# Performance work log

Hardware: AMD Instinct MI355X
Metric: run time of the kernel (lower is better)

## Reference

```python
import jax, jax.numpy as jnp
import numpy as np
from jax import lax

IN_CH = 256
FILTERS_PER_CH = 2            # expansion = 1 -> 2 filters per input channel
INTER_CH = IN_CH * FILTERS_PER_CH
BUTTERFLY_SIZE = 8
BUTTERFLIES = INTER_CH // 2 // BUTTERFLY_SIZE  # 32
WING = BUTTERFLY_SIZE // 2                      # 4


def setup_inputs() -> dict:
    key = jax.random.key(0)
    k1, k2 = jax.random.split(key)
    x = jax.random.normal(k1, (32, IN_CH, 56, 56), dtype=jnp.float32)
    # depthwise conv weight, PyTorch OIHW with groups=IN_CH: (INTER_CH, 1, 3, 3)
    w = jax.random.normal(k2, (INTER_CH, 1, 3, 3), dtype=jnp.float32) * 0.1
    return {"x": x, "w": w}


def reference(x, w):
    # grouped (depthwise, channel multiplier 2) conv, stride 1, pad 1, no bias
    y = lax.conv_general_dilated(
        x, w,
        window_strides=(1, 1),
        padding=[(1, 1), (1, 1)],
        feature_group_count=IN_CH,
        dimension_numbers=("NCHW", "OIHW", "NCHW"),
    )  # (B, INTER_CH, H, W); channels group-major: 2i,2i+1 from input i
    B, C2, H, W = y.shape
    # extract_sequences: consecutive channels alternate between the two outputs
    y = y.reshape(B, C2 // 2, 2, H, W)
    x1 = y[:, :, 0]  # (B, IN_CH, H, W)
    x2 = y[:, :, 1]
    # swap_wings: within each butterfly, swap the two wings
    s = x2.reshape(B, BUTTERFLIES, 2, WING, H, W)
    x2 = jnp.flip(s, axis=2).reshape(B, C2 // 2, H, W)
    return x1 + x2
```

## Files before the change

### kernel.cpp

```cpp
#include <hip/hip_runtime.h>

#define IN_CH 256
#define IMG_W 56
typedef float f4 __attribute__((ext_vector_type(4)));

__global__ __launch_bounds__(448, 5) void dwconv_butterfly(
    const float* __restrict__ x, const float* __restrict__ wgt,
    float* __restrict__ out)
{
    const int tid = threadIdx.x;
    const int pb  = blockIdx.x;
    const int p   = pb & 127;
    const int b   = pb >> 7;
    const int c0  = ((p >> 2) << 3) | (p & 3);
    const int c1  = c0 ^ 4;

    const size_t chan = (size_t)IMG_W * IMG_W;
    const float* x0 = x + ((size_t)b * IN_CH + c0) * chan;
    const float* x1 = x + ((size_t)b * IN_CH + c1) * chan;
    float* o0 = out + ((size_t)b * IN_CH + c0) * chan;
    float* o1 = out + ((size_t)b * IN_CH + c1) * chan;

    const float* pwa = wgt + (size_t)(2 * c0) * 9;
    const float* pwb = wgt + (size_t)(2 * c1 + 1) * 9;
    const float* pwc = wgt + (size_t)(2 * c1) * 9;
    const float* pwd = wgt + (size_t)(2 * c0 + 1) * 9;
    float wa[9], wb[9], wc[9], wd[9];
#pragma unroll
    for (int i = 0; i < 9; ++i) {
        wa[i] = pwa[i]; wb[i] = pwb[i]; wc[i] = pwc[i]; wd[i] = pwd[i];
    }

    if (tid >= 392) return;
    const int s  = tid % 14;
    const int rp = tid / 14;
    const int w0 = 4 * s;
    const bool has_l = (s > 0), has_r = (s < 13);
    const int  col_l = has_l ? w0 - 1 : 0;
    const int  col_r = has_r ? w0 + 4 : IMG_W - 1;

    f4    va[4], vb[4];
    float la[4], ra[4], lb[4], rb[4];
    bool  rv[4];
#pragma unroll
    for (int k = 0; k < 4; ++k) {
        const int ir  = 2 * rp - 1 + k;
        rv[k] = (unsigned)ir < 56u;
        const int irc = ir < 0 ? 0 : (ir > 55 ? 55 : ir);
        const float* r0 = x0 + irc * IMG_W;
        const float* r1 = x1 + irc * IMG_W;
        va[k] = *(const f4*)(r0 + w0);
        vb[k] = *(const f4*)(r1 + w0);
        la[k] = r0[col_l];
        ra[k] = r0[col_r];
        lb[k] = r1[col_l];
        rb[k] = r1[col_r];
    }

    float acc[2][8];
#pragma unroll
    for (int j = 0; j < 2; ++j)
#pragma unroll
        for (int i = 0; i < 8; ++i) acc[j][i] = 0.f;

#pragma unroll
    for (int k = 0; k < 4; ++k) {
        const bool z = !rv[k];
        float W0[6], W1[6];
        W0[0] = (z || !has_l) ? 0.f : la[k];
        W0[1] = z ? 0.f : va[k].x;  W0[2] = z ? 0.f : va[k].y;
        W0[3] = z ? 0.f : va[k].z;  W0[4] = z ? 0.f : va[k].w;
        W0[5] = (z || !has_r) ? 0.f : ra[k];
        W1[0] = (z || !has_l) ? 0.f : lb[k];
        W1[1] = z ? 0.f : vb[k].x;  W1[2] = z ? 0.f : vb[k].y;
        W1[3] = z ? 0.f : vb[k].z;  W1[4] = z ? 0.f : vb[k].w;
        W1[5] = (z || !has_r) ? 0.f : rb[k];
#pragma unroll
        for (int j = 0; j < 2; ++j) {
            const int kh = k - j;
            if (kh < 0 || kh > 2) continue;
#pragma unroll
            for (int kw = 0; kw < 3; ++kw) {
                const float fa = wa[kh * 3 + kw], fb = wb[kh * 3 + kw];
                const float fc = wc[kh * 3 + kw], fd = wd[kh * 3 + kw];
#pragma unroll
                for (int i = 0; i < 4; ++i) {
                    const float u0 = W0[i + kw];
                    const float u1 = W1[i + kw];
                    acc[j][i]     += u0 * fa + u1 * fb;
                    acc[j][4 + i] += u1 * fc + u0 * fd;
                }
            }
        }
    }

#pragma unroll
    for (int j = 0; j < 2; ++j) {
        const int orow = 2 * rp + j;
        f4 v0; v0.x = acc[j][0]; v0.y = acc[j][1]; v0.z = acc[j][2]; v0.w = acc[j][3];
        f4 v1; v1.x = acc[j][4]; v1.y = acc[j][5]; v1.z = acc[j][6]; v1.w = acc[j][7];
        *(f4*)(o0 + orow * IMG_W + w0) = v0;
        *(f4*)(o1 + orow * IMG_W + w0) = v1;
    }
}

extern "C" void kernel_launch(void* const* d_in, const int* in_sizes, int n_in,
                              void* d_out, int out_size, void* d_ws, size_t ws_size,
                              hipStream_t stream) {
    const float* x = (const float*)d_in[0];
    const float* w = (const float*)d_in[1];
    float* out = (float*)d_out;

    dim3 grid(128 * 32);
    dim3 block(448);
    dwconv_butterfly<<<grid, block, 0, stream>>>(x, w, out);
}
```

Baseline: 195.2 us.

## Make waves persistent with double-buffered loads and shuffle-based halo exchange

Each wavefront now handles an 8-row strip of a channel pair and loops over 7 such tiles, prefetching the next tile's inputs and weights into a second register set while computing the current one. The per-thread left and right halo scalar loads are replaced by cross-lane shuffles of neighbouring f4 values. The grid drops to 1024 blocks of 256 threads. The goal is fewer global loads and less block-launch overhead, with load latency overlapping compute. The cost is higher register pressure from the two buffers, 8 of 64 lanes idle per wave, and fewer resident waves to hide latency.

```diff
diff --git a/kernel.cpp b/kernel.cpp
--- a/kernel.cpp
+++ b/kernel.cpp
@@ -2,105 +2,136 @@
 
 #define IN_CH 256
 #define IMG_W 56
+#define CHF   3136
 typedef float f4 __attribute__((ext_vector_type(4)));
 
-__global__ __launch_bounds__(448, 5) void dwconv_butterfly(
+__global__ __launch_bounds__(256, 4) void dwconv_butterfly(
     const float* __restrict__ x, const float* __restrict__ wgt,
     float* __restrict__ out)
 {
-    const int tid = threadIdx.x;
-    const int pb  = blockIdx.x;
-    const int p   = pb & 127;
-    const int b   = pb >> 7;
-    const int c0  = ((p >> 2) << 3) | (p & 3);
-    const int c1  = c0 ^ 4;
+    const int lane = threadIdx.x & 63;
+    const int widx = __builtin_amdgcn_readfirstlane(threadIdx.x >> 6);
+    const int gw   = blockIdx.x * 4 + widx;
+    const int r    = lane / 14;
+    const int s    = lane - r * 14;
+    const bool act   = lane < 56;
+    const int  w0    = 4 * s;
+    const bool has_l = (s > 0), has_r = (s < 13);
 
-    const size_t chan = (size_t)IMG_W * IMG_W;
-    const float* x0 = x + ((size_t)b * IN_CH + c0) * chan;
-    const float* x1 = x + ((size_t)b * IN_CH + c1) * chan;
-    float* o0 = out + ((size_t)b * IN_CH + c0) * chan;
-    float* o1 = out + ((size_t)b * IN_CH + c1) * chan;
+    auto LOAD = [&](int t, f4* va, f4* vb, float* w4) {
+        const int jt = gw + 4096 * t;
+        const int q  = jt % 7;
+        const int pb = jt / 7;
+        const int p  = pb & 127;
+        const int b  = pb >> 7;
+        const int c0 = ((p >> 2) << 3) | (p & 3);
+        const int c1 = c0 ^ 4;
+        const float* x0 = x + ((size_t)b * IN_CH + c0) * CHF;
+        const float* x1 = x + ((size_t)b * IN_CH + c1) * CHF;
+        const int brow = 8 * q + 2 * r - 1;
+        if (act) {
+#pragma unroll
+            for (int k = 0; k < 4; ++k) {
+                const int ir  = brow + k;
+                const int irc = ir < 0 ? 0 : (ir > 55 ? 55 : ir);
+                va[k] = *(const f4*)(x0 + irc * IMG_W + w0);
+                vb[k] = *(const f4*)(x1 + irc * IMG_W + w0);
+            }
+        }
+        const float* pa = wgt + (size_t)(2 * c0) * 9;
+        const float* pq = wgt + (size_t)(2 * c1 + 1) * 9;
+        const float* pc = wgt + (size_t)(2 * c1) * 9;
+        const float* pd = wgt + (size_t)(2 * c0 + 1) * 9;
+#pragma unroll
+        for (int i = 0; i < 9; ++i) {
+            w4[i] = pa[i]; w4[9 + i] = pq[i]; w4[18 + i] = pc[i]; w4[27 + i] = pd[i];
+        }
+    };
 
-    const float* pwa = wgt + (size_t)(2 * c0) * 9;
-    const float* pwb = wgt + (size_t)(2 * c1 + 1) * 9;
-    const float* pwc = wgt + (size_t)(2 * c1) * 9;
-    const float* pwd = wgt + (size_t)(2 * c0 + 1) * 9;
-    float wa[9], wb[9], wc[9], wd[9];
+    auto COMPUTE = [&](int t, f4* va, f4* vb, const float* w4) {
+        const int jt = gw + 4096 * t;
+        const int q  = jt % 7;
+        const int pb = jt / 7;
+        const int p  = pb & 127;
+        const int b  = pb >> 7;
+        const int c0 = ((p >> 2) << 3) | (p & 3);
+        const int c1 = c0 ^ 4;
+        float* o0 = out + ((size_t)b * IN_CH + c0) * CHF;
+        float* o1 = out + ((size_t)b * IN_CH + c1) * CHF;
+        const int brow = 8 * q + 2 * r - 1;
+
+        float acc[2][8];
 #pragma unroll
-    for (int i = 0; i < 9; ++i) {
-        wa[i] = pwa[i]; wb[i] = pwb[i]; wc[i] = pwc[i]; wd[i] = pwd[i];
-    }
-
-    if (tid >= 392) return;
-    const int s  = tid % 14;
-    const int rp = tid / 14;
-    const int w0 = 4 * s;
-    const bool has_l = (s > 0), has_r = (s < 13);
-    const int  col_l = has_l ? w0 - 1 : 0;
-    const int  col_r = has_r ? w0 + 4 : IMG_W - 1;
-
-    f4    va[4], vb[4];
-    float la[4], ra[4], lb[4], rb[4];
-    bool  rv[4];
+        for (int j = 0; j < 2; ++j)
 #pragma unroll
-    for (int k = 0; k < 4; ++k) {
-        const int ir  = 2 * rp - 1 + k;
-        rv[k] = (unsigned)ir < 56u;
-        const int irc = ir < 0 ? 0 : (ir > 55 ? 55 : ir);
-        const float* r0 = x0 + irc * IMG_W;
-        const float* r1 = x1 + irc * IMG_W;
-        va[k] = *(const f4*)(r0 + w0);
-        vb[k] = *(const f4*)(r1 + w0);
-        la[k] = r0[col_l];
-        ra[k] = r0[col_r];
-        lb[k] = r1[col_l];
-        rb[k] = r1[col_r];
-    }
-
-    float acc[2][8];
-#pragma unroll
-    for (int j = 0; j < 2; ++j)
-#pragma unroll
-        for (int i = 0; i < 8; ++i) acc[j][i] = 0.f;
+            for (int i = 0; i < 8; ++i) acc[j][i] = 0.f;
 
 #pragma unroll
-    for (int k = 0; k < 4; ++k) {
-        const bool z = !rv[k];
-        float W0[6], W1[6];
-        W0[0] = (z || !has_l) ? 0.f : la[k];
-        W0[1] = z ? 0.f : va[k].x;  W0[2] = z ? 0.f : va[k].y;
-        W0[3] = z ? 0.f : va[k].z;  W0[4] = z ? 0.f : va[k].w;
-        W0[5] = (z || !has_r) ? 0.f : ra[k];
-        W1[0] = (z || !has_l) ? 0.f : lb[k];
-        W1[1] = z ? 0.f : vb[k].x;  W1[2] = z ? 0.f : vb[k].y;
-        W1[3] = z ? 0.f : vb[k].z;  W1[4] = z ? 0.f : vb[k].w;
-        W1[5] = (z || !has_r) ? 0.f : rb[k];
+        for (int k = 0; k < 4; ++k) {
+            const bool rvk = (unsigned)(brow + k) < 56u;
+            const float lA = __shfl_up(va[k].w, 1);
+            const float rA = __shfl_down(va[k].x, 1);
+            const float lB = __shfl_up(vb[k].w, 1);
+            const float rB = __shfl_down(vb[k].x, 1);
+            float W0[6], W1[6];
+            W0[0] = (rvk && has_l) ? lA : 0.f;
+            W0[1] = rvk ? va[k].x : 0.f;
+            W0[2] = rvk ? va[k].y : 0.f;
+            W0[3] = rvk ? va[k].z : 0.f;
+            W0[4] = rvk ? va[k].w : 0.f;
+            W0[5] = (rvk && has_r) ? rA : 0.f;
+            W1[0] = (rvk && has_l) ? lB : 0.f;
+            W1[1] = rvk ? vb[k].x : 0.f;
+            W1[2] = rvk ? vb[k].y : 0.f;
+            W1[3] = rvk ? vb[k].z : 0.f;
+            W1[4] = rvk ? vb[k].w : 0.f;
+            W1[5] = (rvk && has_r) ? rB : 0.f;
 #pragma unroll
-        for (int j = 0; j < 2; ++j) {
-            const int kh = k - j;
-            if (kh < 0 || kh > 2) continue;
+            for (int j = 0; j < 2; ++j) {
+                const int kh = k - j;
+                if (kh < 0 || kh > 2) continue;
 #pragma unroll
-            for (int kw = 0; kw < 3; ++kw) {
-                const float fa = wa[kh * 3 + kw], fb = wb[kh * 3 + kw];
-                const float fc = wc[kh * 3 + kw], fd = wd[kh * 3 + kw];
+                for (int kw = 0; kw < 3; ++kw) {
+                    const float fa = w4[kh * 3 + kw];
+                    const float fb = w4[9 + kh * 3 + kw];
+                    const float fc = w4[18 + kh * 3 + kw];
+                    const float fd = w4[27 + kh * 3 + kw];
 #pragma unroll
-                for (int i = 0; i < 4; ++i) {
-                    const float u0 = W0[i + kw];
-                    const float u1 = W1[i + kw];
-                    acc[j][i]     += u0 * fa + u1 * fb;
-                    acc[j][4 + i] += u1 * fc + u0 * fd;
+                    for (int i = 0; i < 4; ++i) {
+                        const float u0 = W0[i + kw];
+                        const float u1 = W1[i + kw];
+                        acc[0 + j][i]     += u0 * fa + u1 * fb;
+                        acc[0 + j][4 + i] += u1 * fc + u0 * fd;
+                    }
                 }
             }
         }
-    }
 
+        if (act) {
 #pragma unroll
-    for (int j = 0; j < 2; ++j) {
-        const int orow = 2 * rp + j;
-        f4 v0; v0.x = acc[j][0]; v0.y = acc[j][1]; v0.z = acc[j][2]; v0.w = acc[j][3];
-        f4 v1; v1.x = acc[j][4]; v1.y = acc[j][5]; v1.z = acc[j][6]; v1.w = acc[j][7];
-        *(f4*)(o0 + orow * IMG_W + w0) = v0;
-        *(f4*)(o1 + orow * IMG_W + w0) = v1;
+            for (int j = 0; j < 2; ++j) {
+                const int orow = 8 * q + 2 * r + j;
+                f4 v0; v0.x = acc[j][0]; v0.y = acc[j][1]; v0.z = acc[j][2]; v0.w = acc[j][3];
+                f4 v1; v1.x = acc[j][4]; v1.y = acc[j][5]; v1.z = acc[j][6]; v1.w = acc[j][7];
+                *(f4*)(o0 + orow * IMG_W + w0) = v0;
+                *(f4*)(o1 + orow * IMG_W + w0) = v1;
+            }
+        }
+    };
+
+    f4    vaA[4], vbA[4], vaB[4], vbB[4];
+    float wA[36], wB[36];
+
+    LOAD(0, vaA, vbA, wA);
+#pragma unroll
+    for (int t = 0; t < 7; ++t) {
+        if ((t & 1) == 0) {
+            if (t < 6) LOAD(t + 1, vaB, vbB, wB);
+            COMPUTE(t, vaA, vbA, wA);
+        } else {
+            if (t < 6) LOAD(t + 1, vaA, vbA, wA);
+            COMPUTE(t, vaB, vbB, wB);
+        }
     }
 }
 
@@ -111,7 +142,7 @@
     const float* w = (const float*)d_in[1];
     float* out = (float*)d_out;
 
-    dim3 grid(128 * 32);
-    dim3 block(448);
+    dim3 grid(1024);
+    dim3 block(256);
     dwconv_butterfly<<<grid, block, 0, stream>>>(x, w, out);
 }
```

Result: slower. 235.1 us (+20.4%).
